# Kernel optimization log

Hardware: AMD Instinct MI355X
Metric: run time of the kernel (lower is better)

## Reference

```python
import jax, jax.numpy as jnp
import numpy as np

B, S, H, I, E, TOPK, KS = 4, 4096, 1024, 512, 16, 2, 3


def setup_inputs() -> dict:
    key = jax.random.key(0)
    ks = jax.random.split(key, 9)
    sc = 0.02
    return {
        "hidden_states": jax.random.normal(ks[0], (B, S, H), dtype=jnp.float32),
        "router_w": jax.random.normal(ks[1], (H, E), dtype=jnp.float32) * sc,
        "router_bias": jnp.zeros((E,), dtype=jnp.float32),
        "expert_gate_w": jax.random.normal(ks[2], (E - 1, H, I), dtype=jnp.float32) * sc,
        "expert_up_w": jax.random.normal(ks[3], (E - 1, H, I), dtype=jnp.float32) * sc,
        "expert_down_w": jax.random.normal(ks[4], (E - 1, I, H), dtype=jnp.float32) * sc,
        "conv_w": jax.random.normal(ks[5], (I, H, KS), dtype=jnp.float32) * sc,
        "shared_up_w": jax.random.normal(ks[6], (H, I), dtype=jnp.float32) * sc,
        "shared_down_w": jax.random.normal(ks[7], (I, H), dtype=jnp.float32) * sc,
    }


def reference(hidden_states, router_w, router_bias, expert_gate_w, expert_up_w,
              expert_down_w, conv_w, shared_up_w, shared_down_w):
    b, s, h = hidden_states.shape
    flat = hidden_states.reshape(b * s, h)  # (T, H)

    # ---- Router (mlp type, temperature=1, no noise at eval) ----
    logits = (flat @ router_w).astype(jnp.float32) + router_bias  # (T, E)
    probs = jax.nn.softmax(logits, axis=-1)
    top_w, top_i = jax.lax.top_k(probs, TOPK)  # (T, K)
    norm_w = top_w / (jnp.sum(top_w, axis=-1, keepdims=True) + 1e-6)
    norm_w = norm_w.astype(hidden_states.dtype)
    # Dense combine weights (T, E): scatter top-k weights into expert slots
    combine = jnp.sum(jax.nn.one_hot(top_i, E, dtype=norm_w.dtype) * norm_w[..., None], axis=1)

    # ---- Routed experts: E-1 SwiGLU MLPs + 1 Identity (index E-1) ----
    routed = combine[:, E - 1:E] * flat  # identity expert contribution
    for e in range(E - 1):
        y = (jax.nn.silu(flat @ expert_gate_w[e]) * (flat @ expert_up_w[e])) @ expert_down_w[e]
        routed = routed + combine[:, e:e + 1] * y
    routed = routed.reshape(b, s, h)

    # ---- Shared expert: causal conv1d gate * up, then down ----
    x_ncw = jnp.transpose(hidden_states, (0, 2, 1))  # (B, H, S)
    gate = jax.lax.conv_general_dilated(
        x_ncw, conv_w, window_strides=(1,), padding=[(KS - 1, 0)],
        dimension_numbers=("NCW", "OIW", "NCW"))  # (B, I, S)
    gate = jnp.transpose(gate, (0, 2, 1))  # (B, S, I)
    shared = (jax.nn.silu(gate) * (hidden_states @ shared_up_w)) @ shared_down_w

    return shared + routed
```

## Files before the change

kernel.cpp:

```cpp
#include <hip/hip_runtime.h>

typedef unsigned short u16;
typedef __attribute__((ext_vector_type(4))) float f32x4;
using bf16x8 = __attribute__((ext_vector_type(8))) short;
typedef __attribute__((ext_vector_type(8))) unsigned short u16x8;
typedef __attribute__((ext_vector_type(4))) unsigned short u16x4;

#define GAS __attribute__((address_space(1)))
#define LAS __attribute__((address_space(3)))

__device__ __forceinline__ float bf2f(u16 u) {
  unsigned v = ((unsigned)u) << 16;
  float f;
  __builtin_memcpy(&f, &v, 4);
  return f;
}
__device__ __forceinline__ u16 f2bf(float f) {
  unsigned u;
  __builtin_memcpy(&u, &f, 4);
  u += 0x7fffu + ((u >> 16) & 1u);
  return (u16)(u >> 16);
}
__device__ __forceinline__ void llds16(const void* g, void* l) {
  __builtin_amdgcn_global_load_lds((const GAS unsigned*)g, (LAS unsigned*)l, 16, 0, 0);
}

__global__ void cvtx_k(const float* __restrict__ x, u16* __restrict__ xb) {
  const long i = (long)blockIdx.x * 256 + threadIdx.x;
  f32x4 v = *(const f32x4*)(x + i * 4);
  u16x4 r;
#pragma unroll
  for (int j = 0; j < 4; ++j) r[j] = f2bf(v[j]);
  *(u16x4*)(xb + i * 4) = r;
}

__global__ __launch_bounds__(256) void router_k(const float* __restrict__ x,
    const float* __restrict__ rw, const float* __restrict__ rb,
    int* __restrict__ topk_idx, float* __restrict__ topk_w, int* __restrict__ ib) {
  __shared__ float xs[4][32 * 65];
  __shared__ float wsm[4][32 * 16];
  __shared__ float part[4][64 * 17];
  __shared__ int cnt[16];
  const int tid = threadIdx.x;
  const int wv = __builtin_amdgcn_readfirstlane(tid >> 6);
  const int lane = tid & 63;
  const int tok0 = blockIdx.x * 64;
  const int rr = lane >> 3;
  const int c4 = (lane & 7) * 4;

  float acc[16];
#pragma unroll
  for (int e = 0; e < 16; ++e) acc[e] = 0.f;

  for (int c = 0; c < 8; ++c) {
    const int hb = wv * 256 + c * 32;
    {
      f32x4 wa = *(const f32x4*)(rw + hb * 16 + lane * 4);
      f32x4 wb = *(const f32x4*)(rw + hb * 16 + 256 + lane * 4);
      *(f32x4*)&wsm[wv][lane * 4] = wa;
      *(f32x4*)&wsm[wv][256 + lane * 4] = wb;
    }
#pragma unroll
    for (int i = 0; i < 8; ++i) {
      const int row = i * 8 + rr;
      f32x4 v = *(const f32x4*)(x + (long)(tok0 + row) * 1024 + hb + c4);
#pragma unroll
      for (int j = 0; j < 4; ++j) xs[wv][(c4 + j) * 65 + row] = v[j];
    }
    __syncthreads();
#pragma unroll
    for (int h = 0; h < 32; ++h) {
      const float xv = xs[wv][h * 65 + lane];
      const float* wrow = &wsm[wv][h * 16];
#pragma unroll
      for (int q = 0; q < 4; ++q) {
        f32x4 w4 = *(const f32x4*)(wrow + q * 4);
#pragma unroll
        for (int e = 0; e < 4; ++e) acc[q * 4 + e] += xv * w4[e];
      }
    }
    __syncthreads();
  }
#pragma unroll
  for (int e = 0; e < 16; ++e) part[wv][lane * 17 + e] = acc[e];
  if (tid < 16) cnt[tid] = 0;
  __syncthreads();
  if (tid < 64) {
    float p[16];
#pragma unroll
    for (int e = 0; e < 16; ++e)
      p[e] = part[0][tid * 17 + e] + part[1][tid * 17 + e] +
             part[2][tid * 17 + e] + part[3][tid * 17 + e] + rb[e];
    float mx = p[0];
#pragma unroll
    for (int e = 1; e < 16; ++e) mx = fmaxf(mx, p[e]);
    float sum = 0.f;
#pragma unroll
    for (int e = 0; e < 16; ++e) { p[e] = __expf(p[e] - mx); sum += p[e]; }
    int i0 = 0; float p0 = p[0];
    for (int e = 1; e < 16; ++e) if (p[e] > p0) { p0 = p[e]; i0 = e; }
    int i1 = -1; float p1 = -1.f;
    for (int e = 0; e < 16; ++e) if (e != i0 && p[e] > p1) { p1 = p[e]; i1 = e; }
    const float inv = 1.f / sum;
    p0 *= inv; p1 *= inv;
    const float d = p0 + p1 + 1e-6f;
    const int t = tok0 + tid;
    topk_idx[t * 2] = i0; topk_idx[t * 2 + 1] = i1;
    topk_w[t * 2] = p0 / d;
    topk_w[t * 2 + 1] = p1 / d;
    if (i0 < 15) atomicAdd(&cnt[i0], 1);
    if (i1 < 15) atomicAdd(&cnt[i1], 1);
  }
  __syncthreads();
  if (tid < 15 && cnt[tid] > 0) atomicAdd(&ib[tid], cnt[tid]);
}

__global__ void zero_k(int* __restrict__ ib) {
  if (threadIdx.x < 16) ib[threadIdx.x] = 0;
}

__global__ void scan_k(int* __restrict__ ib) {
  if (threadIdx.x != 0 || blockIdx.x != 0) return;
  int off = 0;
  for (int ee = 0; ee < 15; ++ee) { ib[16 + ee] = off; ib[32 + ee] = off; off += ib[ee]; }
  ib[16 + 15] = off;
  int nm = 0;
  for (int ee = 0; ee < 15; ++ee) {
    const int st = ib[16 + ee], en = ib[16 + ee + 1];
    for (int r = st; r < en; r += 128) {
      ib[64 + nm * 4] = ee; ib[64 + nm * 4 + 1] = r; ib[64 + nm * 4 + 2] = en; ++nm;
    }
  }
  ib[48] = nm;
}

__global__ __launch_bounds__(256) void scatter_k(const int* __restrict__ topk_idx,
                          const float* __restrict__ topk_w,
                          int* __restrict__ ib, int* __restrict__ tok_ids,
                          float* __restrict__ tok_w, int* __restrict__ slot_map) {
  __shared__ int cnt[16], base[16];
  const int tid = threadIdx.x;
  const int j = blockIdx.x * 256 + tid;
  if (tid < 16) cnt[tid] = 0;
  __syncthreads();
  const int e = topk_idx[j];
  int lo = 0;
  if (e < 15) lo = atomicAdd(&cnt[e], 1);
  __syncthreads();
  if (tid < 15 && cnt[tid] > 0) base[tid] = atomicAdd(&ib[32 + tid], cnt[tid]);
  __syncthreads();
  if (e < 15) {
    const int pos = base[e] + lo;
    tok_ids[pos] = j >> 1;
    tok_w[pos] = topk_w[j];
    slot_map[j] = pos;
  } else {
    slot_map[j] = -1;
  }
}

__global__ void transpose_k(const float* __restrict__ src, u16* __restrict__ dst, int R, int C) {
  __shared__ float tile[32][33];
  src += (long)blockIdx.z * R * C;
  dst += (long)blockIdx.z * R * C;
  const int c0 = blockIdx.x * 32, r0 = blockIdx.y * 32;
  const int tx = threadIdx.x & 31, ty = threadIdx.x >> 5;
#pragma unroll
  for (int i = ty; i < 32; i += 8) tile[i][tx] = src[(long)(r0 + i) * C + c0 + tx];
  __syncthreads();
#pragma unroll
  for (int i = ty; i < 32; i += 8) dst[(long)(c0 + i) * R + r0 + tx] = f2bf(tile[tx][i]);
}

__global__ void convt_k(const float* __restrict__ cw, u16* __restrict__ dst) {
  const int idx = blockIdx.x * 256 + threadIdx.x;
  if (idx >= 3 * 512 * 1024) return;
  const int k = idx >> 19;
  const int rem = idx & 524287;
  const int i = rem >> 10, h = rem & 1023;
  dst[idx] = f2bf(cw[i * 3072 + h * 3 + k]);
}

template<int V>
__global__ __launch_bounds__(256, 2)
void gemm_k(const u16* __restrict__ Abase, const u16* __restrict__ Bt0,
            const u16* __restrict__ Bt1, void* __restrict__ OUTv,
            const int* __restrict__ tbl, const int* __restrict__ nmt,
            const int* __restrict__ tok_ids, const float* __restrict__ tok_w,
            int K, int ldA, int ldOut) {
  __shared__ u16 lds[16384];
  u16* OUT = (u16*)OUTv;
  float* OUTF = (float*)OUTv;
  const int tid = threadIdx.x;
  const int wave = tid >> 6, lane = tid & 63;
  const int quad = lane >> 4, l16 = lane & 15;
  const int rA = tid >> 2;
  const int sub8 = (tid & 3) * 8;
  const int sub8s = ((tid & 3) ^ ((tid >> 3) & 3)) * 8;

  constexpr int NYC = (V == 2 || V == 3) ? 4 : 8;
  const int lin = (blockIdx.x & 7) * (gridDim.x >> 3) + (blockIdx.x >> 3);
  const int bx = lin / NYC, by = lin - bx * NYC;

  int e = 0, row0, row_end;
  if constexpr (V <= 1) {
    const int mt = bx;
    if (mt >= *nmt) return;
    e = tbl[mt * 4]; row0 = tbl[mt * 4 + 1]; row_end = tbl[mt * 4 + 2];
  } else {
    row0 = bx * 128; row_end = row0 + 128;
  }
  const int n0 = by * ((V == 0) ? 64 : 128);

  f32x4 acc[2][8];
#pragma unroll
  for (int i = 0; i < 2; ++i)
#pragma unroll
    for (int j = 0; j < 8; ++j) acc[i][j] = (f32x4){0.f, 0.f, 0.f, 0.f};

  const int swz8 = (((l16 >> 1) & 3) ^ quad) * 8;
  const int aoff0 = (wave * 32 + l16) * 32 + swz8;
  const int aoff1 = aoff0 + 512;

  int cur = 0;
  u16x8 va0n, va1n;

  const int nph = (V == 3) ? 3 : 1;
  const int kIters = K / 32;
  for (int ph = 0; ph < nph; ++ph) {
    const u16 *pA0, *pA1, *pB0, *pB1;
    bool zero0 = false;
    if constexpr (V == 0) {
      const int t0i = tok_ids[min(row0 + rA, row_end - 1)];
      const int t1i = tok_ids[min(row0 + rA + 64, row_end - 1)];
      pA0 = Abase + (long)t0i * 1024 + sub8s;
      pA1 = Abase + (long)t1i * 1024 + sub8s;
      pB0 = Bt0 + ((long)e * 512 + n0 + rA) * 1024 + sub8s;
      pB1 = Bt1 + ((long)e * 512 + n0 + rA) * 1024 + sub8s;
    } else if constexpr (V == 1) {
      pA0 = Abase + (long)min(row0 + rA, row_end - 1) * 512 + sub8s;
      pA1 = Abase + (long)min(row0 + rA + 64, row_end - 1) * 512 + sub8s;
      pB0 = Bt0 + ((long)e * 1024 + n0 + rA) * 512 + sub8s;
      pB1 = Bt0 + ((long)e * 1024 + n0 + rA + 64) * 512 + sub8s;
    } else if constexpr (V == 2 || V == 4) {
      pA0 = Abase + (long)(row0 + rA) * ldA + sub8s;
      pA1 = Abase + (long)(row0 + rA + 64) * ldA + sub8s;
      pB0 = Bt0 + (long)(n0 + rA) * K + sub8s;
      pB1 = Bt0 + (long)(n0 + rA + 64) * K + sub8s;
    } else {
      const int bb = row0 >> 12, s0 = row0 & 4095;
      const int si0 = s0 + ph - 2 + rA;
      zero0 = si0 < 0;
      pA0 = Abase + ((long)bb * 4096 + (si0 < 0 ? 0 : si0)) * 1024 + sub8s;
      pA1 = Abase + ((long)bb * 4096 + (si0 + 64)) * 1024 + sub8s;
      pB0 = Bt0 + (long)ph * 512 * 1024 + (long)(n0 + rA) * 1024 + sub8s;
      pB1 = Bt0 + (long)ph * 512 * 1024 + (long)(n0 + rA + 64) * 1024 + sub8s;
    }

    if constexpr (V == 3) {
      va0n = *(const u16x8*)pA0; pA0 += 32;
      va1n = *(const u16x8*)pA1; pA1 += 32;
      if (zero0) va0n = (u16x8){0, 0, 0, 0, 0, 0, 0, 0};
      *(u16x8*)&lds[cur + rA * 32 + sub8] = va0n;
      *(u16x8*)&lds[cur + (rA + 64) * 32 + sub8] = va1n;
    } else {
      llds16(pA0, &lds[cur + wave * 512]); pA0 += 32;
      llds16(pA1, &lds[cur + 2048 + wave * 512]); pA1 += 32;
    }
    llds16(pB0, &lds[cur + 4096 + wave * 512]); pB0 += 32;
    llds16(pB1, &lds[cur + 6144 + wave * 512]); pB1 += 32;
    __syncthreads();

    for (int kb = 0; kb < kIters; ++kb) {
      const int nxt = cur ^ 8192;
      const bool pre = (kb + 1 < kIters);
      if constexpr (V == 3) {
        if (pre) {
          llds16(pB0, &lds[nxt + 4096 + wave * 512]); pB0 += 32;
          llds16(pB1, &lds[nxt + 6144 + wave * 512]); pB1 += 32;
          va0n = *(const u16x8*)pA0; pA0 += 32;
          va1n = *(const u16x8*)pA1; pA1 += 32;
          if (zero0) va0n = (u16x8){0, 0, 0, 0, 0, 0, 0, 0};
        }
      } else {
        if (pre) {
          llds16(pA0, &lds[nxt + wave * 512]); pA0 += 32;
          llds16(pA1, &lds[nxt + 2048 + wave * 512]); pA1 += 32;
          llds16(pB0, &lds[nxt + 4096 + wave * 512]); pB0 += 32;
          llds16(pB1, &lds[nxt + 6144 + wave * 512]); pB1 += 32;
        }
      }
      bf16x8 a0 = *(const bf16x8*)&lds[cur + aoff0];
      bf16x8 a1 = *(const bf16x8*)&lds[cur + aoff1];
#pragma unroll
      for (int nt = 0; nt < 8; ++nt) {
        bf16x8 b = *(const bf16x8*)&lds[cur + 4096 + (nt * 16 + l16) * 32 + swz8];
        acc[0][nt] = __builtin_amdgcn_mfma_f32_16x16x32_bf16(a0, b, acc[0][nt], 0, 0, 0);
        acc[1][nt] = __builtin_amdgcn_mfma_f32_16x16x32_bf16(a1, b, acc[1][nt], 0, 0, 0);
      }
      if constexpr (V == 3) {
        if (pre) {
          *(u16x8*)&lds[nxt + rA * 32 + sub8] = va0n;
          *(u16x8*)&lds[nxt + (rA + 64) * 32 + sub8] = va1n;
        }
      }
      __syncthreads();
      cur = nxt;
    }
  }

  const int rbase = wave * 32;
  if constexpr (V == 0) {
#pragma unroll
    for (int mt = 0; mt < 2; ++mt)
#pragma unroll
      for (int r = 0; r < 4; ++r) {
        const int row = rbase + mt * 16 + quad * 4 + r;
#pragma unroll
        for (int nt = 0; nt < 4; ++nt) {
          float g = acc[mt][nt][r], u = acc[mt][nt + 4][r];
          float sg = g / (1.f + __expf(-g));
          lds[row * 64 + nt * 16 + l16] = f2bf(sg * u);
        }
      }
    __syncthreads();
#pragma unroll
    for (int i = 0; i < 4; ++i) {
      const int c = i * 256 + tid;
      const int row = c >> 3, s8 = (c & 7) * 8;
      const int slot = row0 + row;
      if (slot < row_end)
        *(u16x8*)(OUT + (long)slot * ldOut + n0 + s8) = *(const u16x8*)&lds[row * 64 + s8];
    }
  } else if constexpr (V == 1) {
#pragma unroll
    for (int mt = 0; mt < 2; ++mt)
#pragma unroll
      for (int r = 0; r < 4; ++r) {
        const int row = rbase + mt * 16 + quad * 4 + r;
        const float wgt = tok_w[min(row0 + row, row_end - 1)];
#pragma unroll
        for (int nt = 0; nt < 8; ++nt)
          lds[row * 128 + nt * 16 + l16] = f2bf(acc[mt][nt][r] * wgt);
      }
    __syncthreads();
#pragma unroll
    for (int i = 0; i < 8; ++i) {
      const int c = i * 256 + tid;
      const int row = c >> 4, s8 = (c & 15) * 8;
      const int slot = row0 + row;
      if (slot < row_end)
        *(u16x8*)(OUT + (long)slot * ldOut + n0 + s8) = *(const u16x8*)&lds[row * 128 + s8];
    }
  } else if constexpr (V == 2) {
#pragma unroll
    for (int mt = 0; mt < 2; ++mt)
#pragma unroll
      for (int r = 0; r < 4; ++r) {
        const int row = rbase + mt * 16 + quad * 4 + r;
#pragma unroll
        for (int nt = 0; nt < 8; ++nt)
          lds[row * 128 + nt * 16 + l16] = f2bf(acc[mt][nt][r]);
      }
    __syncthreads();
#pragma unroll
    for (int i = 0; i < 8; ++i) {
      const int c = i * 256 + tid;
      const int row = c >> 4, s8 = (c & 15) * 8;
      *(u16x8*)(OUT + (long)(row0 + row) * ldOut + n0 + s8) = *(const u16x8*)&lds[row * 128 + s8];
    }
  } else if constexpr (V == 3) {
#pragma unroll
    for (int mt = 0; mt < 2; ++mt)
#pragma unroll
      for (int r = 0; r < 4; ++r) {
        const int row = rbase + mt * 16 + quad * 4 + r;
#pragma unroll
        for (int nt = 0; nt < 8; ++nt) {
          float g = acc[mt][nt][r];
          lds[row * 128 + nt * 16 + l16] = f2bf(g / (1.f + __expf(-g)));
        }
      }
    __syncthreads();
#pragma unroll
    for (int i = 0; i < 8; ++i) {
      const int c = i * 256 + tid;
      const int row = c >> 4, s8 = (c & 15) * 8;
      const long o = (long)(row0 + row) * ldOut + n0 + s8;
      u16x8 sg8 = *(const u16x8*)&lds[row * 128 + s8];
      u16x8 up8 = *(const u16x8*)(OUT + o);
      u16x8 res;
#pragma unroll
      for (int j = 0; j < 8; ++j) res[j] = f2bf(bf2f(sg8[j]) * bf2f(up8[j]));
      *(u16x8*)(OUT + o) = res;
    }
  } else {
#pragma unroll
    for (int mt = 0; mt < 2; ++mt)
#pragma unroll
      for (int r = 0; r < 4; ++r) {
        const int row = row0 + rbase + mt * 16 + quad * 4 + r;
#pragma unroll
        for (int nt = 0; nt < 8; ++nt)
          OUTF[(long)row * ldOut + n0 + nt * 16 + l16] = acc[mt][nt][r];
      }
  }
}

__global__ void final_k(const float* __restrict__ x, const u16* __restrict__ Y,
                        const int* __restrict__ slot_map, const float* __restrict__ topk_w,
                        float* __restrict__ out) {
  const long idx = (long)blockIdx.x * 256 + threadIdx.x;
  const int t = (int)(idx >> 8), cc = ((int)idx & 255) * 4;
  const long ob = (long)t * 1024 + cc;
  f32x4 o = *(const f32x4*)(out + ob);
#pragma unroll
  for (int k2 = 0; k2 < 2; ++k2) {
    const int sm = slot_map[t * 2 + k2];
    if (sm >= 0) {
      u16x4 y = *(const u16x4*)(Y + (long)sm * 1024 + cc);
#pragma unroll
      for (int j = 0; j < 4; ++j) o[j] += bf2f(y[j]);
    } else {
      const float w = topk_w[t * 2 + k2];
      f32x4 xv = *(const f32x4*)(x + ob);
#pragma unroll
      for (int j = 0; j < 4; ++j) o[j] += w * xv[j];
    }
  }
  *(f32x4*)(out + ob) = o;
}

extern "C" void kernel_launch(void* const* d_in, const int* in_sizes, int n_in,
                              void* d_out, int out_size, void* d_ws, size_t ws_size,
                              hipStream_t stream) {
  (void)in_sizes; (void)n_in; (void)out_size; (void)ws_size;
  const float* x   = (const float*)d_in[0];
  const float* rw  = (const float*)d_in[1];
  const float* rb  = (const float*)d_in[2];
  const float* gw  = (const float*)d_in[3];
  const float* uw  = (const float*)d_in[4];
  const float* dw  = (const float*)d_in[5];
  const float* cw  = (const float*)d_in[6];
  const float* suw = (const float*)d_in[7];
  const float* sdw = (const float*)d_in[8];
  float* out = (float*)d_out;

  char* base = (char*)d_ws;
  size_t off = 0;
  auto alloc = [&](size_t b) { void* p = base + off; off = (off + b + 255) & ~(size_t)255; return p; };
  u16* xb     = (u16*)alloc(16777216ull * 2);
  u16* gate_t = (u16*)alloc(15ull * 512 * 1024 * 2);
  u16* up_t   = (u16*)alloc(15ull * 512 * 1024 * 2);
  u16* down_t = (u16*)alloc(15ull * 1024 * 512 * 2);
  u16* conv_t = (u16*)alloc(3ull * 512 * 1024 * 2);
  u16* sup_t  = (u16*)alloc(512ull * 1024 * 2);
  u16* sdn_t  = (u16*)alloc(512ull * 1024 * 2);
  u16* inter  = (u16*)alloc(32768ull * 512 * 2);
  u16* Y      = (u16*)alloc(32768ull * 1024 * 2);
  u16* UP     = (u16*)alloc(16384ull * 512 * 2);
  int*   topi    = (int*)alloc(32768 * 4);
  float* topw    = (float*)alloc(32768 * 4);
  int*   smap    = (int*)alloc(32768 * 4);
  int*   tok_ids = (int*)alloc(32768 * 4);
  float* tokw    = (float*)alloc(32768 * 4);
  int*   ib      = (int*)alloc(8192);

  zero_k<<<1, 64, 0, stream>>>(ib);
  cvtx_k<<<16384, 256, 0, stream>>>(x, xb);
  transpose_k<<<dim3(16, 32, 15), 256, 0, stream>>>(gw, gate_t, 1024, 512);
  transpose_k<<<dim3(16, 32, 15), 256, 0, stream>>>(uw, up_t, 1024, 512);
  transpose_k<<<dim3(32, 16, 15), 256, 0, stream>>>(dw, down_t, 512, 1024);
  transpose_k<<<dim3(16, 32, 1), 256, 0, stream>>>(suw, sup_t, 1024, 512);
  transpose_k<<<dim3(32, 16, 1), 256, 0, stream>>>(sdw, sdn_t, 512, 1024);
  convt_k<<<6144, 256, 0, stream>>>(cw, conv_t);
  router_k<<<256, 256, 0, stream>>>(x, rw, rb, topi, topw, ib);
  scan_k<<<1, 64, 0, stream>>>(ib);
  scatter_k<<<128, 256, 0, stream>>>(topi, topw, ib, tok_ids, tokw, smap);
  gemm_k<0><<<2176, 256, 0, stream>>>(xb, gate_t, up_t, inter, ib + 64, ib + 48,
                                      tok_ids, tokw, 1024, 1024, 512);
  gemm_k<1><<<2176, 256, 0, stream>>>(inter, down_t, nullptr, Y, ib + 64, ib + 48,
                                      nullptr, tokw, 512, 512, 1024);
  gemm_k<2><<<512, 256, 0, stream>>>(xb, sup_t, nullptr, UP, nullptr, nullptr,
                                     nullptr, nullptr, 1024, 1024, 512);
  gemm_k<3><<<512, 256, 0, stream>>>(xb, conv_t, nullptr, UP, nullptr, nullptr,
                                     nullptr, nullptr, 1024, 1024, 512);
  gemm_k<4><<<1024, 256, 0, stream>>>(UP, sdn_t, nullptr, out, nullptr, nullptr,
                                      nullptr, nullptr, 512, 512, 1024);
  final_k<<<16384, 256, 0, stream>>>(x, Y, smap, topw, out);
}
```

Baseline: 572.7 us.

## Enlarge GEMM block tiles to 256 rows with a 2x2 wave layout

All GEMM variants now use 256-row M tiles instead of 128. The four waves are arranged 2x2, each computing a 128xN/2 sub-tile with 8x4 MFMA accumulators, and the expert tile table steps by 256 rows. The goal is to reuse each loaded B tile across twice as many rows and raise MFMA work per LDS read, cutting global and LDS traffic. In exchange it uses more LDS and registers per block, which may lower occupancy, and it adds more padding waste on partially filled per-expert tiles.

```diff
diff --git a/kernel.cpp b/kernel.cpp
--- a/kernel.cpp
+++ b/kernel.cpp
@@ -127,7 +127,7 @@
   int nm = 0;
   for (int ee = 0; ee < 15; ++ee) {
     const int st = ib[16 + ee], en = ib[16 + ee + 1];
-    for (int r = st; r < en; r += 128) {
+    for (int r = st; r < en; r += 256) {
       ib[64 + nm * 4] = ee; ib[64 + nm * 4 + 1] = r; ib[64 + nm * 4 + 2] = en; ++nm;
     }
   }
@@ -188,12 +188,13 @@
             const int* __restrict__ tbl, const int* __restrict__ nmt,
             const int* __restrict__ tok_ids, const float* __restrict__ tok_w,
             int K, int ldA, int ldOut) {
-  __shared__ u16 lds[16384];
+  __shared__ u16 lds[24576];
   u16* OUT = (u16*)OUTv;
   float* OUTF = (float*)OUTv;
   const int tid = threadIdx.x;
   const int wave = tid >> 6, lane = tid & 63;
   const int quad = lane >> 4, l16 = lane & 15;
+  const int wm = wave >> 1, wn = wave & 1;
   const int rA = tid >> 2;
   const int sub8 = (tid & 3) * 8;
   const int sub8s = ((tid & 3) ^ ((tid >> 3) & 3)) * 8;
@@ -204,205 +205,241 @@
 
   int e = 0, row0, row_end;
   if constexpr (V <= 1) {
-    const int mt = bx;
-    if (mt >= *nmt) return;
-    e = tbl[mt * 4]; row0 = tbl[mt * 4 + 1]; row_end = tbl[mt * 4 + 2];
+    if (bx >= *nmt) return;
+    e = tbl[bx * 4]; row0 = tbl[bx * 4 + 1]; row_end = tbl[bx * 4 + 2];
   } else {
-    row0 = bx * 128; row_end = row0 + 128;
+    row0 = bx * 256; row_end = row0 + 256;
   }
   const int n0 = by * ((V == 0) ? 64 : 128);
 
-  f32x4 acc[2][8];
-#pragma unroll
-  for (int i = 0; i < 2; ++i)
-#pragma unroll
-    for (int j = 0; j < 8; ++j) acc[i][j] = (f32x4){0.f, 0.f, 0.f, 0.f};
+  f32x4 acc[8][4];
+#pragma unroll
+  for (int i = 0; i < 8; ++i)
+#pragma unroll
+    for (int j = 0; j < 4; ++j) acc[i][j] = (f32x4){0.f, 0.f, 0.f, 0.f};
 
   const int swz8 = (((l16 >> 1) & 3) ^ quad) * 8;
-  const int aoff0 = (wave * 32 + l16) * 32 + swz8;
-  const int aoff1 = aoff0 + 512;
+  const int aob = (wm * 128 + l16) * 32 + swz8;
+  int bof[4];
+#pragma unroll
+  for (int n = 0; n < 4; ++n) {
+    const int brow = (V == 0) ? (wn * 32 + (n & 1) * 16 + (n >> 1) * 64)
+                              : (wn * 64 + n * 16);
+    bof[n] = 8192 + (brow + l16) * 32 + swz8;
+  }
 
   int cur = 0;
-  u16x8 va0n, va1n;
-
-  const int nph = (V == 3) ? 3 : 1;
   const int kIters = K / 32;
-  for (int ph = 0; ph < nph; ++ph) {
-    const u16 *pA0, *pA1, *pB0, *pB1;
-    bool zero0 = false;
+
+  if constexpr (V != 3) {
+    const u16 *pA0, *pA1, *pA2, *pA3, *pB0, *pB1;
     if constexpr (V == 0) {
-      const int t0i = tok_ids[min(row0 + rA, row_end - 1)];
-      const int t1i = tok_ids[min(row0 + rA + 64, row_end - 1)];
-      pA0 = Abase + (long)t0i * 1024 + sub8s;
-      pA1 = Abase + (long)t1i * 1024 + sub8s;
+      const int t0 = tok_ids[min(row0 + rA, row_end - 1)];
+      const int t1 = tok_ids[min(row0 + rA + 64, row_end - 1)];
+      const int t2 = tok_ids[min(row0 + rA + 128, row_end - 1)];
+      const int t3 = tok_ids[min(row0 + rA + 192, row_end - 1)];
+      pA0 = Abase + (long)t0 * 1024 + sub8s;
+      pA1 = Abase + (long)t1 * 1024 + sub8s;
+      pA2 = Abase + (long)t2 * 1024 + sub8s;
+      pA3 = Abase + (long)t3 * 1024 + sub8s;
       pB0 = Bt0 + ((long)e * 512 + n0 + rA) * 1024 + sub8s;
       pB1 = Bt1 + ((long)e * 512 + n0 + rA) * 1024 + sub8s;
     } else if constexpr (V == 1) {
       pA0 = Abase + (long)min(row0 + rA, row_end - 1) * 512 + sub8s;
       pA1 = Abase + (long)min(row0 + rA + 64, row_end - 1) * 512 + sub8s;
+      pA2 = Abase + (long)min(row0 + rA + 128, row_end - 1) * 512 + sub8s;
+      pA3 = Abase + (long)min(row0 + rA + 192, row_end - 1) * 512 + sub8s;
       pB0 = Bt0 + ((long)e * 1024 + n0 + rA) * 512 + sub8s;
       pB1 = Bt0 + ((long)e * 1024 + n0 + rA + 64) * 512 + sub8s;
-    } else if constexpr (V == 2 || V == 4) {
+    } else {
       pA0 = Abase + (long)(row0 + rA) * ldA + sub8s;
       pA1 = Abase + (long)(row0 + rA + 64) * ldA + sub8s;
+      pA2 = Abase + (long)(row0 + rA + 128) * ldA + sub8s;
+      pA3 = Abase + (long)(row0 + rA + 192) * ldA + sub8s;
       pB0 = Bt0 + (long)(n0 + rA) * K + sub8s;
       pB1 = Bt0 + (long)(n0 + rA + 64) * K + sub8s;
-    } else {
+    }
+    auto STAGE = [&](int buf) {
+      llds16(pA0, &lds[buf + wave * 512]); pA0 += 32;
+      llds16(pA1, &lds[buf + 2048 + wave * 512]); pA1 += 32;
+      llds16(pA2, &lds[buf + 4096 + wave * 512]); pA2 += 32;
+      llds16(pA3, &lds[buf + 6144 + wave * 512]); pA3 += 32;
+      llds16(pB0, &lds[buf + 8192 + wave * 512]); pB0 += 32;
+      llds16(pB1, &lds[buf + 10240 + wave * 512]); pB1 += 32;
+    };
+    STAGE(cur);
+    __syncthreads();
+    for (int kb = 0; kb < kIters; ++kb) {
+      const int nxt = cur ^ 12288;
+      if (kb + 1 < kIters) STAGE(nxt);
+      bf16x8 b0 = *(const bf16x8*)&lds[cur + bof[0]];
+      bf16x8 b1 = *(const bf16x8*)&lds[cur + bof[1]];
+      bf16x8 b2 = *(const bf16x8*)&lds[cur + bof[2]];
+      bf16x8 b3 = *(const bf16x8*)&lds[cur + bof[3]];
+#pragma unroll
+      for (int m = 0; m < 8; ++m) {
+        bf16x8 a = *(const bf16x8*)&lds[cur + aob + m * 512];
+        acc[m][0] = __builtin_amdgcn_mfma_f32_16x16x32_bf16(a, b0, acc[m][0], 0, 0, 0);
+        acc[m][1] = __builtin_amdgcn_mfma_f32_16x16x32_bf16(a, b1, acc[m][1], 0, 0, 0);
+        acc[m][2] = __builtin_amdgcn_mfma_f32_16x16x32_bf16(a, b2, acc[m][2], 0, 0, 0);
+        acc[m][3] = __builtin_amdgcn_mfma_f32_16x16x32_bf16(a, b3, acc[m][3], 0, 0, 0);
+      }
+      __syncthreads();
+      cur = nxt;
+    }
+  } else {
+    u16x8 va0, va1, va2, va3;
+    for (int ph = 0; ph < 3; ++ph) {
       const int bb = row0 >> 12, s0 = row0 & 4095;
       const int si0 = s0 + ph - 2 + rA;
-      zero0 = si0 < 0;
-      pA0 = Abase + ((long)bb * 4096 + (si0 < 0 ? 0 : si0)) * 1024 + sub8s;
-      pA1 = Abase + ((long)bb * 4096 + (si0 + 64)) * 1024 + sub8s;
-      pB0 = Bt0 + (long)ph * 512 * 1024 + (long)(n0 + rA) * 1024 + sub8s;
-      pB1 = Bt0 + (long)ph * 512 * 1024 + (long)(n0 + rA + 64) * 1024 + sub8s;
-    }
-
-    if constexpr (V == 3) {
-      va0n = *(const u16x8*)pA0; pA0 += 32;
-      va1n = *(const u16x8*)pA1; pA1 += 32;
-      if (zero0) va0n = (u16x8){0, 0, 0, 0, 0, 0, 0, 0};
-      *(u16x8*)&lds[cur + rA * 32 + sub8] = va0n;
-      *(u16x8*)&lds[cur + (rA + 64) * 32 + sub8] = va1n;
-    } else {
-      llds16(pA0, &lds[cur + wave * 512]); pA0 += 32;
-      llds16(pA1, &lds[cur + 2048 + wave * 512]); pA1 += 32;
-    }
-    llds16(pB0, &lds[cur + 4096 + wave * 512]); pB0 += 32;
-    llds16(pB1, &lds[cur + 6144 + wave * 512]); pB1 += 32;
+      const bool zero0 = si0 < 0;
+      const u16* pA0 = Abase + ((long)bb * 4096 + (si0 < 0 ? 0 : si0)) * 1024 + sub8s;
+      const u16* pA1 = Abase + ((long)bb * 4096 + (si0 + 64)) * 1024 + sub8s;
+      const u16* pA2 = Abase + ((long)bb * 4096 + (si0 + 128)) * 1024 + sub8s;
+      const u16* pA3 = Abase + ((long)bb * 4096 + (si0 + 192)) * 1024 + sub8s;
+      const u16* pB0 = Bt0 + (long)ph * 524288 + (long)(n0 + rA) * 1024 + sub8s;
+      const u16* pB1 = Bt0 + (long)ph * 524288 + (long)(n0 + rA + 64) * 1024 + sub8s;
+
+      va0 = *(const u16x8*)pA0; pA0 += 32;
+      va1 = *(const u16x8*)pA1; pA1 += 32;
+      va2 = *(const u16x8*)pA2; pA2 += 32;
+      va3 = *(const u16x8*)pA3; pA3 += 32;
+      if (zero0) va0 = (u16x8){0, 0, 0, 0, 0, 0, 0, 0};
+      *(u16x8*)&lds[cur + rA * 32 + sub8] = va0;
+      *(u16x8*)&lds[cur + (rA + 64) * 32 + sub8] = va1;
+      *(u16x8*)&lds[cur + (rA + 128) * 32 + sub8] = va2;
+      *(u16x8*)&lds[cur + (rA + 192) * 32 + sub8] = va3;
+      llds16(pB0, &lds[cur + 8192 + wave * 512]); pB0 += 32;
+      llds16(pB1, &lds[cur + 10240 + wave * 512]); pB1 += 32;
+      __syncthreads();
+
+      for (int kb = 0; kb < kIters; ++kb) {
+        const int nxt = cur ^ 12288;
+        const bool pre = (kb + 1 < kIters);
+        if (pre) {
+          llds16(pB0, &lds[nxt + 8192 + wave * 512]); pB0 += 32;
+          llds16(pB1, &lds[nxt + 10240 + wave * 512]); pB1 += 32;
+          va0 = *(const u16x8*)pA0; pA0 += 32;
+          va1 = *(const u16x8*)pA1; pA1 += 32;
+          va2 = *(const u16x8*)pA2; pA2 += 32;
+          va3 = *(const u16x8*)pA3; pA3 += 32;
+          if (zero0) va0 = (u16x8){0, 0, 0, 0, 0, 0, 0, 0};
+        }
+        bf16x8 b0 = *(const bf16x8*)&lds[cur + bof[0]];
+        bf16x8 b1 = *(const bf16x8*)&lds[cur + bof[1]];
+        bf16x8 b2 = *(const bf16x8*)&lds[cur + bof[2]];
+        bf16x8 b3 = *(const bf16x8*)&lds[cur + bof[3]];
+#pragma unroll
+        for (int m = 0; m < 8; ++m) {
+          bf16x8 a = *(const bf16x8*)&lds[cur + aob + m * 512];
+          acc[m][0] = __builtin_amdgcn_mfma_f32_16x16x32_bf16(a, b0, acc[m][0], 0, 0, 0);
+          acc[m][1] = __builtin_amdgcn_mfma_f32_16x16x32_bf16(a, b1, acc[m][1], 0, 0, 0);
+          acc[m][2] = __builtin_amdgcn_mfma_f32_16x16x32_bf16(a, b2, acc[m][2], 0, 0, 0);
+          acc[m][3] = __builtin_amdgcn_mfma_f32_16x16x32_bf16(a, b3, acc[m][3], 0, 0, 0);
+        }
+        if (pre) {
+          *(u16x8*)&lds[nxt + rA * 32 + sub8] = va0;
+          *(u16x8*)&lds[nxt + (rA + 64) * 32 + sub8] = va1;
+          *(u16x8*)&lds[nxt + (rA + 128) * 32 + sub8] = va2;
+          *(u16x8*)&lds[nxt + (rA + 192) * 32 + sub8] = va3;
+        }
+        __syncthreads();
+        cur = nxt;
+      }
+    }
+  }
+
+  if constexpr (V == 0) {
+#pragma unroll
+    for (int m = 0; m < 8; ++m)
+#pragma unroll
+      for (int r = 0; r < 4; ++r) {
+        const int row = wm * 128 + m * 16 + quad * 4 + r;
+#pragma unroll
+        for (int n = 0; n < 2; ++n) {
+          float g = acc[m][n][r], u = acc[m][n + 2][r];
+          float sg = g / (1.f + __expf(-g));
+          lds[row * 64 + wn * 32 + n * 16 + l16] = f2bf(sg * u);
+        }
+      }
     __syncthreads();
-
-    for (int kb = 0; kb < kIters; ++kb) {
-      const int nxt = cur ^ 8192;
-      const bool pre = (kb + 1 < kIters);
-      if constexpr (V == 3) {
-        if (pre) {
-          llds16(pB0, &lds[nxt + 4096 + wave * 512]); pB0 += 32;
-          llds16(pB1, &lds[nxt + 6144 + wave * 512]); pB1 += 32;
-          va0n = *(const u16x8*)pA0; pA0 += 32;
-          va1n = *(const u16x8*)pA1; pA1 += 32;
-          if (zero0) va0n = (u16x8){0, 0, 0, 0, 0, 0, 0, 0};
-        }
-      } else {
-        if (pre) {
-          llds16(pA0, &lds[nxt + wave * 512]); pA0 += 32;
-          llds16(pA1, &lds[nxt + 2048 + wave * 512]); pA1 += 32;
-          llds16(pB0, &lds[nxt + 4096 + wave * 512]); pB0 += 32;
-          llds16(pB1, &lds[nxt + 6144 + wave * 512]); pB1 += 32;
-        }
-      }
-      bf16x8 a0 = *(const bf16x8*)&lds[cur + aoff0];
-      bf16x8 a1 = *(const bf16x8*)&lds[cur + aoff1];
-#pragma unroll
-      for (int nt = 0; nt < 8; ++nt) {
-        bf16x8 b = *(const bf16x8*)&lds[cur + 4096 + (nt * 16 + l16) * 32 + swz8];
-        acc[0][nt] = __builtin_amdgcn_mfma_f32_16x16x32_bf16(a0, b, acc[0][nt], 0, 0, 0);
-        acc[1][nt] = __builtin_amdgcn_mfma_f32_16x16x32_bf16(a1, b, acc[1][nt], 0, 0, 0);
-      }
-      if constexpr (V == 3) {
-        if (pre) {
-          *(u16x8*)&lds[nxt + rA * 32 + sub8] = va0n;
-          *(u16x8*)&lds[nxt + (rA + 64) * 32 + sub8] = va1n;
-        }
-      }
-      __syncthreads();
-      cur = nxt;
-    }
-  }
-
-  const int rbase = wave * 32;
-  if constexpr (V == 0) {
-#pragma unroll
-    for (int mt = 0; mt < 2; ++mt)
-#pragma unroll
-      for (int r = 0; r < 4; ++r) {
-        const int row = rbase + mt * 16 + quad * 4 + r;
-#pragma unroll
-        for (int nt = 0; nt < 4; ++nt) {
-          float g = acc[mt][nt][r], u = acc[mt][nt + 4][r];
-          float sg = g / (1.f + __expf(-g));
-          lds[row * 64 + nt * 16 + l16] = f2bf(sg * u);
-        }
-      }
-    __syncthreads();
-#pragma unroll
-    for (int i = 0; i < 4; ++i) {
+#pragma unroll
+    for (int i = 0; i < 8; ++i) {
       const int c = i * 256 + tid;
       const int row = c >> 3, s8 = (c & 7) * 8;
       const int slot = row0 + row;
       if (slot < row_end)
         *(u16x8*)(OUT + (long)slot * ldOut + n0 + s8) = *(const u16x8*)&lds[row * 64 + s8];
     }
-  } else if constexpr (V == 1) {
-#pragma unroll
-    for (int mt = 0; mt < 2; ++mt)
+  } else if constexpr (V == 1 || V == 2) {
+#pragma unroll
+    for (int p = 0; p < 2; ++p) {
+      if (p) __syncthreads();
+#pragma unroll
+      for (int mm = 0; mm < 4; ++mm) {
+        const int m = p * 4 + mm;
+#pragma unroll
+        for (int r = 0; r < 4; ++r) {
+          const int grow = row0 + wm * 128 + m * 16 + quad * 4 + r;
+          float wgt = 1.f;
+          if constexpr (V == 1) wgt = tok_w[min(grow, row_end - 1)];
+          const int row2 = wm * 64 + mm * 16 + quad * 4 + r;
+#pragma unroll
+          for (int n = 0; n < 4; ++n)
+            lds[row2 * 128 + wn * 64 + n * 16 + l16] = f2bf(acc[m][n][r] * wgt);
+        }
+      }
+      __syncthreads();
+#pragma unroll
+      for (int i = 0; i < 8; ++i) {
+        const int c = i * 256 + tid;
+        const int row2 = c >> 4, s8 = (c & 15) * 8;
+        const int gr = row0 + (row2 >> 6) * 128 + (row2 & 63) + p * 64;
+        if (V == 2 || gr < row_end)
+          *(u16x8*)(OUT + (long)gr * ldOut + n0 + s8) = *(const u16x8*)&lds[row2 * 128 + s8];
+      }
+    }
+  } else if constexpr (V == 3) {
+#pragma unroll
+    for (int p = 0; p < 2; ++p) {
+      if (p) __syncthreads();
+#pragma unroll
+      for (int mm = 0; mm < 4; ++mm) {
+        const int m = p * 4 + mm;
+#pragma unroll
+        for (int r = 0; r < 4; ++r) {
+          const int row2 = wm * 64 + mm * 16 + quad * 4 + r;
+#pragma unroll
+          for (int n = 0; n < 4; ++n) {
+            float g = acc[m][n][r];
+            lds[row2 * 128 + wn * 64 + n * 16 + l16] = f2bf(g / (1.f + __expf(-g)));
+          }
+        }
+      }
+      __syncthreads();
+#pragma unroll
+      for (int i = 0; i < 8; ++i) {
+        const int c = i * 256 + tid;
+        const int row2 = c >> 4, s8 = (c & 15) * 8;
+        const int gr = row0 + (row2 >> 6) * 128 + (row2 & 63) + p * 64;
+        const long o = (long)gr * ldOut + n0 + s8;
+        u16x8 sg8 = *(const u16x8*)&lds[row2 * 128 + s8];
+        u16x8 up8 = *(const u16x8*)(OUT + o);
+        u16x8 res;
+#pragma unroll
+        for (int j = 0; j < 8; ++j) res[j] = f2bf(bf2f(sg8[j]) * bf2f(up8[j]));
+        *(u16x8*)(OUT + o) = res;
+      }
+    }
+  } else {
+#pragma unroll
+    for (int m = 0; m < 8; ++m)
 #pragma unroll
       for (int r = 0; r < 4; ++r) {
-        const int row = rbase + mt * 16 + quad * 4 + r;
-        const float wgt = tok_w[min(row0 + row, row_end - 1)];
-#pragma unroll
-        for (int nt = 0; nt < 8; ++nt)
-          lds[row * 128 + nt * 16 + l16] = f2bf(acc[mt][nt][r] * wgt);
-      }
-    __syncthreads();
-#pragma unroll
-    for (int i = 0; i < 8; ++i) {
-      const int c = i * 256 + tid;
-      const int row = c >> 4, s8 = (c & 15) * 8;
-      const int slot = row0 + row;
-      if (slot < row_end)
-        *(u16x8*)(OUT + (long)slot * ldOut + n0 + s8) = *(const u16x8*)&lds[row * 128 + s8];
-    }
-  } else if constexpr (V == 2) {
-#pragma unroll
-    for (int mt = 0; mt < 2; ++mt)
-#pragma unroll
-      for (int r = 0; r < 4; ++r) {
-        const int row = rbase + mt * 16 + quad * 4 + r;
-#pragma unroll
-        for (int nt = 0; nt < 8; ++nt)
-          lds[row * 128 + nt * 16 + l16] = f2bf(acc[mt][nt][r]);
-      }
-    __syncthreads();
-#pragma unroll
-    for (int i = 0; i < 8; ++i) {
-      const int c = i * 256 + tid;
-      const int row = c >> 4, s8 = (c & 15) * 8;
-      *(u16x8*)(OUT + (long)(row0 + row) * ldOut + n0 + s8) = *(const u16x8*)&lds[row * 128 + s8];
-    }
-  } else if constexpr (V == 3) {
-#pragma unroll
-    for (int mt = 0; mt < 2; ++mt)
-#pragma unroll
-      for (int r = 0; r < 4; ++r) {
-        const int row = rbase + mt * 16 + quad * 4 + r;
-#pragma unroll
-        for (int nt = 0; nt < 8; ++nt) {
-          float g = acc[mt][nt][r];
-          lds[row * 128 + nt * 16 + l16] = f2bf(g / (1.f + __expf(-g)));
-        }
-      }
-    __syncthreads();
-#pragma unroll
-    for (int i = 0; i < 8; ++i) {
-      const int c = i * 256 + tid;
-      const int row = c >> 4, s8 = (c & 15) * 8;
-      const long o = (long)(row0 + row) * ldOut + n0 + s8;
-      u16x8 sg8 = *(const u16x8*)&lds[row * 128 + s8];
-      u16x8 up8 = *(const u16x8*)(OUT + o);
-      u16x8 res;
-#pragma unroll
-      for (int j = 0; j < 8; ++j) res[j] = f2bf(bf2f(sg8[j]) * bf2f(up8[j]));
-      *(u16x8*)(OUT + o) = res;
-    }
-  } else {
-#pragma unroll
-    for (int mt = 0; mt < 2; ++mt)
-#pragma unroll
-      for (int r = 0; r < 4; ++r) {
-        const int row = row0 + rbase + mt * 16 + quad * 4 + r;
-#pragma unroll
-        for (int nt = 0; nt < 8; ++nt)
-          OUTF[(long)row * ldOut + n0 + nt * 16 + l16] = acc[mt][nt][r];
+        const int row = row0 + wm * 128 + m * 16 + quad * 4 + r;
+#pragma unroll
+        for (int n = 0; n < 4; ++n)
+          OUTF[(long)row * ldOut + n0 + wn * 64 + n * 16 + l16] = acc[m][n][r];
       }
   }
 }
@@ -477,15 +514,15 @@
   router_k<<<256, 256, 0, stream>>>(x, rw, rb, topi, topw, ib);
   scan_k<<<1, 64, 0, stream>>>(ib);
   scatter_k<<<128, 256, 0, stream>>>(topi, topw, ib, tok_ids, tokw, smap);
-  gemm_k<0><<<2176, 256, 0, stream>>>(xb, gate_t, up_t, inter, ib + 64, ib + 48,
+  gemm_k<0><<<1152, 256, 0, stream>>>(xb, gate_t, up_t, inter, ib + 64, ib + 48,
                                       tok_ids, tokw, 1024, 1024, 512);
-  gemm_k<1><<<2176, 256, 0, stream>>>(inter, down_t, nullptr, Y, ib + 64, ib + 48,
+  gemm_k<1><<<1152, 256, 0, stream>>>(inter, down_t, nullptr, Y, ib + 64, ib + 48,
                                       nullptr, tokw, 512, 512, 1024);
-  gemm_k<2><<<512, 256, 0, stream>>>(xb, sup_t, nullptr, UP, nullptr, nullptr,
+  gemm_k<2><<<256, 256, 0, stream>>>(xb, sup_t, nullptr, UP, nullptr, nullptr,
                                      nullptr, nullptr, 1024, 1024, 512);
-  gemm_k<3><<<512, 256, 0, stream>>>(xb, conv_t, nullptr, UP, nullptr, nullptr,
+  gemm_k<3><<<256, 256, 0, stream>>>(xb, conv_t, nullptr, UP, nullptr, nullptr,
                                      nullptr, nullptr, 1024, 1024, 512);
-  gemm_k<4><<<1024, 256, 0, stream>>>(UP, sdn_t, nullptr, out, nullptr, nullptr,
-                                      nullptr, nullptr, 512, 512, 1024);
+  gemm_k<4><<<512, 256, 0, stream>>>(UP, sdn_t, nullptr, out, nullptr, nullptr,
+                                     nullptr, nullptr, 512, 512, 1024);
   final_k<<<16384, 256, 0, stream>>>(x, Y, smap, topw, out);
 }
```

Result: slower. 593.7 us (+3.7%).
